# Optimization experiments

Measured on AMD Instinct MI355X. Metric: run time of the kernel, lower is better.

Reference implementation:

```python
import jax, jax.numpy as jnp
import numpy as np

NDIM = 1024
NTOKEN = 50257
CUTOFFS = [2000, 10000, NTOKEN]  # cutoffs + [ntoken]
DIV = 4
N = 4096
HEAD_SIZE = CUTOFFS[0] + len(CUTOFFS) - 1  # 2002


def setup_inputs() -> dict:
    key = jax.random.key(0)
    ks = jax.random.split(key, 8)
    inputs = jax.random.normal(ks[0], (N, NDIM), dtype=jnp.float32)
    targets = jax.random.randint(ks[1], (N,), 0, NTOKEN, dtype=jnp.int32)
    # head: nn.Linear(ndim, head_size, bias=False) -> weight [head_size, ndim], xavier
    def xavier(k, shape):
        fan_out, fan_in = shape
        lim = np.sqrt(6.0 / (fan_in + fan_out))
        return jax.random.uniform(k, shape, jnp.float32, -lim, lim)
    head_W = xavier(ks[2], (HEAD_SIZE, NDIM))
    # tail cluster 0: size 8000, low dim 256; cluster 1: size 40257, low dim 64
    sz0 = CUTOFFS[1] - CUTOFFS[0]
    sz1 = CUTOFFS[2] - CUTOFFS[1]
    d0, d1 = NDIM // DIV, NDIM // DIV**2
    emb0 = jax.random.normal(ks[3], (sz0, d0), dtype=jnp.float32) * d0 ** -0.5
    emb1 = jax.random.normal(ks[4], (sz1, d1), dtype=jnp.float32) * d1 ** -0.5
    lin0 = xavier(ks[5], (NDIM, d0))  # nn.Linear(d0, ndim).weight
    lin1 = xavier(ks[6], (NDIM, d1))
    return {"inputs": inputs, "targets": targets, "head_W": head_W,
            "emb0": emb0, "lin0": lin0, "emb1": emb1, "lin1": lin1}


def _adaptive_logprob(inputs, targets, head_W, emb0, lin0, emb1, lin1):
    tails = [(emb0, lin0), (emb1, lin1)]
    # map targets -> head targets (in-head id, or cluster slot cutoffs[0]+i)
    head_targets = targets
    masks = []
    for i in range(len(tails)):
        m = (targets >= CUTOFFS[i]) & (targets < CUTOFFS[i + 1])
        masks.append(m)
        head_targets = jnp.where(m, CUTOFFS[0] + i, head_targets)
    # head: logits [N, head_size], gather per-row log-prob
    head_lp = jax.nn.log_softmax(inputs @ head_W.T, axis=-1)
    out = jnp.take_along_axis(head_lp, head_targets[:, None], axis=1)[:, 0]
    # tails: logits = (x @ lin) @ emb^T (low-rank), log-softmax, masked gather
    for i, (emb, lin) in enumerate(tails):
        size = CUTOFFS[i + 1] - CUTOFFS[i]
        lp = jax.nn.log_softmax((inputs @ lin) @ emb.T, axis=-1)  # [N, size]
        rel = jnp.clip(targets - CUTOFFS[i], 0, size - 1)
        g = jnp.take_along_axis(lp, rel[:, None], axis=1)[:, 0]
        out = out + jnp.where(masks[i], g, 0.0)
    return out


def reference(inputs, targets, head_W, emb0, lin0, emb1, lin1):
    outputs = _adaptive_logprob(inputs, targets, head_W, emb0, lin0, emb1, lin1)
    loss = (-outputs).mean()
    return outputs, loss
```

## Files before the change

### kernel.cpp

```cpp
#include <hip/hip_runtime.h>


typedef __attribute__((ext_vector_type(8))) short short8;
typedef __attribute__((ext_vector_type(4))) float f32x4;

#define LOG2E 1.4426950408889634f
#define LN2   0.6931471805599453f

__device__ __forceinline__ float b2f(unsigned short u){
    return __uint_as_float(((unsigned int)u) << 16);
}
__device__ __forceinline__ unsigned short f2b(float f){
    unsigned int x = __float_as_uint(f);
    x += 0x7fffu + ((x >> 16) & 1u);
    return (unsigned short)(x >> 16);
}
__device__ __forceinline__ float dotu(unsigned int xu, unsigned int wu){
    float a = __uint_as_float(xu << 16) * __uint_as_float(wu << 16);
    float b = __uint_as_float(xu & 0xffff0000u) * __uint_as_float(wu & 0xffff0000u);
    return a + b;
}
__device__ __forceinline__ float fexp2(float x){
#if __has_builtin(__builtin_amdgcn_exp2f)
    return __builtin_amdgcn_exp2f(x);
#else
    float r; asm("v_exp_f32 %0, %1" : "=v"(r) : "v"(x)); return r;
#endif
}

__global__ __launch_bounds__(256) void k_prep(
    const float* __restrict__ X, const float* __restrict__ headW,
    const float* __restrict__ emb0, const float* __restrict__ emb1,
    const float* __restrict__ lin0, const float* __restrict__ lin1,
    unsigned short* __restrict__ Xb, unsigned short* __restrict__ hWb,
    unsigned short* __restrict__ e0b, unsigned short* __restrict__ e1b,
    unsigned short* __restrict__ l0T, unsigned short* __restrict__ l1T,
    float* __restrict__ sums)
{
    __shared__ unsigned short tileT[64][65];
    const int b = blockIdx.x, t = threadIdx.x;
    if (b < 80){
        const float* src; unsigned short* dst; int C, tx, ty;
        if (b < 64){ src = lin0; dst = l0T; C = 256; tx = b & 3; ty = b >> 2; }
        else       { src = lin1; dst = l1T; C = 64;  tx = 0;     ty = b - 64; }
        #pragma unroll
        for (int e = 0; e < 16; ++e){
            int idx = t + e*256, r = idx >> 6, c = idx & 63;
            tileT[c][r] = f2b(src[(ty*64 + r)*C + tx*64 + c]);
        }
        __syncthreads();
        #pragma unroll
        for (int e = 0; e < 16; ++e){
            int idx = t + e*256, cc = idx >> 6, rr = idx & 63;
            dst[(tx*64 + cc)*1024 + ty*64 + rr] = tileT[cc][rr];
        }
        return;
    }
    const int NX = 1048576, NH = 512512, NE0 = 512000, NE1 = 644112;
    const int NV = NX + NH + NE0 + NE1;
    const int NS = 12288;
    const int total = NV + NS;
    int stride = (gridDim.x - 80) * blockDim.x;
    for (int i = (b - 80)*blockDim.x + t; i < total; i += stride){
        if (i < NV){
            const float* src; unsigned short* dst; int off; float sc;
            if (i < NX)            { src = X;     dst = Xb;  off = i;           sc = 1.0f;  }
            else if (i < NX+NH)    { src = headW; dst = hWb; off = i-NX;        sc = LOG2E; }
            else if (i < NX+NH+NE0){ src = emb0;  dst = e0b; off = i-NX-NH;     sc = LOG2E; }
            else                   { src = emb1;  dst = e1b; off = i-NX-NH-NE0; sc = LOG2E; }
            float4 v = ((const float4*)src)[off];
            ushort4 o;
            o.x = f2b(v.x*sc); o.y = f2b(v.y*sc);
            o.z = f2b(v.z*sc); o.w = f2b(v.w*sc);
            ((ushort4*)dst)[off] = o;
        } else {
            sums[i - NV] = 0.f;
        }
    }
}

__global__ __launch_bounds__(256) void k_hgemm(
    const unsigned short* __restrict__ A,
    const unsigned short* __restrict__ B0, unsigned short* __restrict__ C0,
    const unsigned short* __restrict__ B1, unsigned short* __restrict__ C1)
{
    constexpr int K = 1024;
    __shared__ __align__(16) unsigned short As[64*64];
    __shared__ __align__(16) unsigned short Bs[64*64];

    const int yy = blockIdx.y;
    const unsigned short* B = (yy < 4) ? B0 : B1;
    unsigned short* C = (yy < 4) ? C0 : C1;
    const int M  = (yy < 4) ? 256 : 64;
    const int cb = (yy < 4) ? yy : 0;

    const int tid  = threadIdx.x;
    const int lane = tid & 63;
    const int w    = tid >> 6;
    const int waveR = w >> 1, waveC = w & 1;
    const int quad  = lane >> 4, l16 = lane & 15;
    const int row0  = blockIdx.x * 64;

    f32x4 acc[2][2];
    #pragma unroll
    for (int i = 0; i < 2; ++i)
    #pragma unroll
    for (int j = 0; j < 2; ++j)
        acc[i][j] = (f32x4){0.f, 0.f, 0.f, 0.f};

    for (int kc = 0; kc < K/64; ++kc){
        __syncthreads();
        #pragma unroll
        for (int it = 0; it < 2; ++it){
            int idx = tid + it*256;
            int r = idx >> 3, g = idx & 7;
            *((uint4*)&As[r*64 + ((g ^ (r & 7)) << 3)]) =
                *(const uint4*)(A + (row0 + r)*K + kc*64 + g*8);
            *((uint4*)&Bs[r*64 + ((g ^ (r & 7)) << 3)]) =
                *(const uint4*)(B + (cb*64 + r)*K + kc*64 + g*8);
        }
        __syncthreads();
        #pragma unroll
        for (int ks = 0; ks < 2; ++ks){
            short8 a[2], b[2];
            #pragma unroll
            for (int i = 0; i < 2; ++i){
                int r = waveR*32 + i*16 + l16;
                int g = ks*4 + quad;
                a[i] = *(const short8*)&As[r*64 + ((g ^ (r & 7)) << 3)];
            }
            #pragma unroll
            for (int j = 0; j < 2; ++j){
                int r = waveC*32 + j*16 + l16;
                int g = ks*4 + quad;
                b[j] = *(const short8*)&Bs[r*64 + ((g ^ (r & 7)) << 3)];
            }
            #pragma unroll
            for (int i = 0; i < 2; ++i)
            #pragma unroll
            for (int j = 0; j < 2; ++j)
                acc[i][j] = __builtin_amdgcn_mfma_f32_16x16x32_bf16(
                    a[i], b[j], acc[i][j], 0, 0, 0);
        }
    }
    #pragma unroll
    for (int i = 0; i < 2; ++i)
    #pragma unroll
    for (int j = 0; j < 2; ++j)
    #pragma unroll
    for (int r = 0; r < 4; ++r){
        int row = row0 + waveR*32 + i*16 + quad*4 + r;
        int col = cb*64 + waveC*32 + j*16 + l16;
        C[row*M + col] = f2b(acc[i][j][r]);
    }
}

template<int K>
__device__ __forceinline__ void sumexp_lds(
    const unsigned short* __restrict__ A,
    const unsigned short* __restrict__ B,
    float* __restrict__ s_out, int M,
    int rowb, int cb0, int cb1,
    unsigned short* __restrict__ As,
    unsigned short* __restrict__ Bs)
{
    constexpr int KCH = K / 64;
    constexpr int LK  = (KCH == 16) ? 4 : 2;
    static_assert(KCH == 16 || KCH == 4, "");
    const int tid  = threadIdx.x;
    const int lane = tid & 63, w = tid >> 6;
    const int waveR = w >> 1, waveC = w & 1;
    const int quad  = lane >> 4, l16 = lane & 15;
    const int row0  = rowb * 64;
    const int nit   = (cb1 - cb0) << LK;

    float s_loc[8];
    #pragma unroll
    for (int i = 0; i < 8; ++i) s_loc[i] = 0.f;
    f32x4 acc[2][2];
    #pragma unroll
    for (int i = 0; i < 2; ++i)
    #pragma unroll
    for (int j = 0; j < 2; ++j) acc[i][j] = (f32x4){0.f,0.f,0.f,0.f};

    const int srow = tid >> 3;
    const int sg   = tid & 7;
    const int so0 = srow*64 + ((sg ^ (srow & 7)) << 3);
    const int so1 = (srow+32)*64 + ((sg ^ ((srow+32) & 7)) << 3);

    int aoff[2][2], boff[2][2];
    #pragma unroll
    for (int x = 0; x < 2; ++x)
    #pragma unroll
    for (int ks = 0; ks < 2; ++ks){
        int ra = waveR*32 + x*16 + l16;
        int rb = waveC*32 + x*16 + l16;
        int g  = ks*4 + quad;
        aoff[x][ks] = ra*64 + ((g ^ (ra & 7)) << 3);
        boff[x][ks] = rb*64 + ((g ^ (rb & 7)) << 3);
    }

    uint4 A0a, A1a, B0a, B1a, A0b, A1b, B0b, B1b;
    auto loadAB = [&](int it, uint4& A0, uint4& A1, uint4& B0, uint4& B1){
        int cb = cb0 + (it >> LK);
        int kc = it & (KCH - 1);
        const unsigned short* ap = A + (row0 + srow)*K + kc*64 + sg*8;
        A0 = *(const uint4*)ap;
        A1 = *(const uint4*)(ap + 32*K);
        int br = cb*64 + srow;
        const unsigned short* bp = B + br*K + kc*64 + sg*8;
        B0 = (br      < M) ? *(const uint4*)bp          : (uint4){0,0,0,0};
        B1 = (br + 32 < M) ? *(const uint4*)(bp + 32*K) : (uint4){0,0,0,0};
    };
    auto writeAB = [&](int it, uint4 A0, uint4 A1, uint4 B0, uint4 B1){
        unsigned short* Ad = As + (it & 1)*4096;
        unsigned short* Bd = Bs + (it & 1)*4096;
        *(uint4*)(Ad + so0) = A0; *(uint4*)(Ad + so1) = A1;
        *(uint4*)(Bd + so0) = B0; *(uint4*)(Bd + so1) = B1;
    };
    auto compute = [&](int buf){
        const unsigned short* Ac = As + buf*4096;
        const unsigned short* Bc = Bs + buf*4096;
        #pragma unroll
        for (int ks = 0; ks < 2; ++ks){
            short8 a0 = *(const short8*)(Ac + aoff[0][ks]);
            short8 a1 = *(const short8*)(Ac + aoff[1][ks]);
            short8 b0 = *(const short8*)(Bc + boff[0][ks]);
            short8 b1 = *(const short8*)(Bc + boff[1][ks]);
            acc[0][0] = __builtin_amdgcn_mfma_f32_16x16x32_bf16(a0, b0, acc[0][0], 0,0,0);
            acc[0][1] = __builtin_amdgcn_mfma_f32_16x16x32_bf16(a0, b1, acc[0][1], 0,0,0);
            acc[1][0] = __builtin_amdgcn_mfma_f32_16x16x32_bf16(a1, b0, acc[1][0], 0,0,0);
            acc[1][1] = __builtin_amdgcn_mfma_f32_16x16x32_bf16(a1, b1, acc[1][1], 0,0,0);
        }
    };
    auto epilogue = [&](int it){
        int cb = cb0 + (it >> LK);
        if ((cb + 1)*64 <= M){
            #pragma unroll
            for (int i = 0; i < 2; ++i)
            #pragma unroll
            for (int j = 0; j < 2; ++j)
            #pragma unroll
            for (int r = 0; r < 4; ++r)
                s_loc[i*4 + r] += fexp2(acc[i][j][r]);
        } else {
            #pragma unroll
            for (int j = 0; j < 2; ++j){
                int col = cb*64 + waveC*32 + j*16 + l16;
                if (col < M){
                    #pragma unroll
                    for (int i = 0; i < 2; ++i)
                    #pragma unroll
                    for (int r = 0; r < 4; ++r)
                        s_loc[i*4 + r] += fexp2(acc[i][j][r]);
                }
            }
        }
        #pragma unroll
        for (int i = 0; i < 2; ++i)
        #pragma unroll
        for (int j = 0; j < 2; ++j) acc[i][j] = (f32x4){0.f,0.f,0.f,0.f};
    };

    loadAB(0, A0a, A1a, B0a, B1a);
    writeAB(0, A0a, A1a, B0a, B1a);
    loadAB(1, A0b, A1b, B0b, B1b);
    loadAB(2, A0a, A1a, B0a, B1a);
    __syncthreads();

    for (int it = 0; it < nit; it += 2){
        writeAB(it + 1, A0b, A1b, B0b, B1b);
        if (it + 3 < nit) loadAB(it + 3, A0b, A1b, B0b, B1b);
        compute(0);
        __syncthreads();
        if (it + 2 < nit) writeAB(it + 2, A0a, A1a, B0a, B1a);
        if (it + 4 < nit) loadAB(it + 4, A0a, A1a, B0a, B1a);
        compute(1);
        if (((it + 1) & (KCH - 1)) == (KCH - 1)) epilogue(it + 1);
        __syncthreads();
    }

    #pragma unroll
    for (int k = 0; k < 8; ++k){
        #pragma unroll
        for (int m = 1; m < 16; m <<= 1)
            s_loc[k] += __shfl_xor(s_loc[k], m, 64);
    }
    if (l16 < 8){
        int i = l16 >> 2, r = l16 & 3;
        int row = row0 + waveR*32 + i*16 + quad*4 + r;
        atomicAdd(&s_out[row], s_loc[l16]);
    }
}

__device__ __forceinline__ void sumexp_stream64(
    const unsigned short* __restrict__ A,
    const unsigned short* __restrict__ B,
    float* __restrict__ s_out, int wid)
{
    const int M = 40257;
    const int lane = threadIdx.x & 63;
    const int quad = lane >> 4, l16 = lane & 15;
    const int rowg  = wid >> 6;
    const int split = wid & 63;
    const int g0 = split*39 + min(split, 21);
    const int g1 = g0 + 39 + (split < 21 ? 1 : 0);
    const int row0 = rowg * 64;

    short8 a[4][2];
    #pragma unroll
    for (int i = 0; i < 4; ++i)
    #pragma unroll
    for (int ks = 0; ks < 2; ++ks)
        a[i][ks] = *(const short8*)(A + (row0 + i*16 + l16)*64 + ks*32 + quad*8);

    f32x4 sums[4];
    #pragma unroll
    for (int i = 0; i < 4; ++i) sums[i] = (f32x4){0.f,0.f,0.f,0.f};

    short8 p0a, p1a, p0b, p1b;
    auto loadB = [&](int g, short8& d0, short8& d1){
        int n = g*16 + l16; if (n > M-1) n = M-1;
        const unsigned short* p = B + n*64 + quad*8;
        d0 = *(const short8*)p;
        d1 = *(const short8*)(p + 32);
    };
    auto body = [&](int g, short8 b0, short8 b1){
        f32x4 acc[4];
        #pragma unroll
        for (int i = 0; i < 4; ++i) acc[i] = (f32x4){0.f,0.f,0.f,0.f};
        #pragma unroll
        for (int i = 0; i < 4; ++i)
            acc[i] = __builtin_amdgcn_mfma_f32_16x16x32_bf16(a[i][0], b0, acc[i], 0,0,0);
        #pragma unroll
        for (int i = 0; i < 4; ++i)
            acc[i] = __builtin_amdgcn_mfma_f32_16x16x32_bf16(a[i][1], b1, acc[i], 0,0,0);
        if (g*16 + l16 < M){
            #pragma unroll
            for (int i = 0; i < 4; ++i){
                sums[i][0] += fexp2(acc[i][0]);
                sums[i][1] += fexp2(acc[i][1]);
                sums[i][2] += fexp2(acc[i][2]);
                sums[i][3] += fexp2(acc[i][3]);
            }
        }
    };

    loadB(g0, p0a, p1a);
    loadB(g0 + 1, p0b, p1b);
    for (int g = g0; g < g1; g += 2){
        body(g, p0a, p1a);
        if (g + 2 < g1) loadB(g + 2, p0a, p1a);
        if (g + 1 < g1){
            body(g + 1, p0b, p1b);
            if (g + 3 < g1) loadB(g + 3, p0b, p1b);
        }
    }

    #pragma unroll
    for (int i = 0; i < 4; ++i){
        #pragma unroll
        for (int r = 0; r < 4; ++r){
            float v = sums[i][r];
            v += __shfl_xor(v, 1, 64);
            v += __shfl_xor(v, 2, 64);
            v += __shfl_xor(v, 4, 64);
            v += __shfl_xor(v, 8, 64);
            if (l16 == 0)
                atomicAdd(&s_out[row0 + i*16 + quad*4 + r], v);
        }
    }
}

__global__ __launch_bounds__(256) void k_sumexp(
    const unsigned short* __restrict__ Xb,  const unsigned short* __restrict__ hWb,
    const unsigned short* __restrict__ h0b, const unsigned short* __restrict__ e0b,
    const unsigned short* __restrict__ h1b, const unsigned short* __restrict__ e1b,
    float* __restrict__ sH, float* __restrict__ s0, float* __restrict__ s1)
{
    __shared__ __align__(16) unsigned short As[2*4096];
    __shared__ __align__(16) unsigned short Bs[2*4096];
    const int b = blockIdx.x;
    const int m4 = b & 3;
    if (m4 == 0){
        int id = b >> 2, rowb = id >> 3, split = id & 7;
        sumexp_lds<1024>(Xb, hWb, sH, 2002, rowb, split*4, split*4 + 4, As, Bs);
    } else if (m4 == 2){
        int id = b >> 2, rowb = id >> 3, split = id & 7;
        int cb0 = split*15 + min(split, 5);
        int cb1 = cb0 + 15 + (split < 5 ? 1 : 0);
        sumexp_lds<256>(h0b, e0b, s0, 8000, rowb, cb0, cb1, As, Bs);
    } else {
        int wid = (b >> 1)*4 + (threadIdx.x >> 6);
        sumexp_stream64(h1b, e1b, s1, wid);
    }
}

__global__ __launch_bounds__(256) void k_combine(
    const unsigned short* __restrict__ Xb,
    const unsigned short* __restrict__ hWb,
    const unsigned short* __restrict__ h0b,
    const unsigned short* __restrict__ e0b,
    const unsigned short* __restrict__ h1b,
    const unsigned short* __restrict__ e1b,
    const float* __restrict__ sH, const float* __restrict__ s0,
    const float* __restrict__ s1,
    const int* __restrict__ targets, float* __restrict__ out)
{
    int w = threadIdx.x >> 6, lane = threadIdx.x & 63;
    int row = blockIdx.x*4 + w;
    int t = targets[row];
    int hidx = t < 2000 ? t : (t < 10000 ? 2000 : 2001);
    int rel0 = min(max(t - 2000, 0), 7999);
    int rel1 = min(max(t - 10000, 0), 40256);

    float dh = 0.f;
    {
        const uint4* xa = (const uint4*)(Xb  + row*1024  + lane*16);
        const uint4* wb = (const uint4*)(hWb + hidx*1024 + lane*16);
        #pragma unroll
        for (int p = 0; p < 2; ++p){
            uint4 xv = xa[p], wv = wb[p];
            dh += dotu(xv.x, wv.x) + dotu(xv.y, wv.y)
                + dotu(xv.z, wv.z) + dotu(xv.w, wv.w);
        }
    }
    float d0;
    {
        uint2 xv = *(const uint2*)(h0b + row*256  + lane*4);
        uint2 wv = *(const uint2*)(e0b + rel0*256 + lane*4);
        d0 = dotu(xv.x, wv.x) + dotu(xv.y, wv.y);
    }
    float d1 = b2f(h1b[row*64 + lane]) * b2f(e1b[rel1*64 + lane]);

    #pragma unroll
    for (int m = 1; m < 64; m <<= 1){
        dh += __shfl_xor(dh, m, 64);
        d0 += __shfl_xor(d0, m, 64);
        d1 += __shfl_xor(d1, m, 64);
    }
    if (lane == 0){
        float lp = dh - log2f(sH[row]);
        if (t >= 2000 && t < 10000) lp += d0 - log2f(s0[row]);
        if (t >= 10000)             lp += d1 - log2f(s1[row]);
        out[row] = LN2 * lp;
    }
}

__global__ void k_loss(const float* __restrict__ out, float* __restrict__ loss){
    __shared__ float red[1024];
    float s = 0.f;
    for (int i = threadIdx.x; i < 4096; i += 1024) s += out[i];
    red[threadIdx.x] = s;
    __syncthreads();
    for (int ofs = 512; ofs > 0; ofs >>= 1){
        if (threadIdx.x < ofs) red[threadIdx.x] += red[threadIdx.x + ofs];
        __syncthreads();
    }
    if (threadIdx.x == 0) loss[0] = -red[0] / 4096.f;
}

extern "C" void kernel_launch(void* const* d_in, const int* in_sizes, int n_in,
                              void* d_out, int out_size, void* d_ws, size_t ws_size,
                              hipStream_t stream) {
    const float* X      = (const float*)d_in[0];
    const int*   tgt    = (const int*)  d_in[1];
    const float* headW  = (const float*)d_in[2];
    const float* emb0   = (const float*)d_in[3];
    const float* lin0   = (const float*)d_in[4];
    const float* emb1   = (const float*)d_in[5];
    const float* lin1   = (const float*)d_in[6];
    float* out = (float*)d_out;

    char* ws = (char*)d_ws;
    unsigned short* Xb  = (unsigned short*)(ws + 0);
    unsigned short* hWb = (unsigned short*)(ws + 8388608);
    unsigned short* e0b = (unsigned short*)(ws + 12488704);
    unsigned short* e1b = (unsigned short*)(ws + 16584704);
    unsigned short* l0T = (unsigned short*)(ws + 21737600);
    unsigned short* l1T = (unsigned short*)(ws + 22261888);
    unsigned short* h0b = (unsigned short*)(ws + 22392960);
    unsigned short* h1b = (unsigned short*)(ws + 24490112);
    float* sums         = (float*)(ws + 25014400);
    float* sH = sums, *s0 = sums + 4096, *s1 = sums + 8192;

    k_prep<<<2048, 256, 0, stream>>>(X, headW, emb0, emb1, lin0, lin1,
                                     Xb, hWb, e0b, e1b, l0T, l1T, sums);
    k_hgemm<<<dim3(64, 5), 256, 0, stream>>>(Xb, l0T, h0b, l1T, h1b);
    k_sumexp<<<2048, 256, 0, stream>>>(Xb, hWb, h0b, e0b, h1b, e1b, sH, s0, s1);
    k_combine<<<1024, 256, 0, stream>>>(Xb, hWb, h0b, e0b, h1b, e1b,
                                        sH, s0, s1, tgt, out);
    k_loss<<<1, 1024, 0, stream>>>(out, out + 4096);
}
```

Before: 234.2 us.

## Use 128x128 MFMA tiles with direct global-to-LDS loads in GEMM and sum-exp kernels

Grows the block tile in the projection GEMM and the head and tail-0 sum-exp kernels from 64x64 to 128x128, so each wave runs a 4x4 grid of MFMA tiles. The LDS tiles are now filled with global_load_lds instead of going through registers. The projection GEMM now reads lin0 and lin1 as one 320-row matrix, which relies on the two buffers sitting next to each other in the workspace. The tail-1 streaming path now covers 128 rows per wave, and the work split and grid sizes are recomputed to match. The goal is more operand reuse and less global and LDS staging traffic per FLOP. In exchange it drops the earlier register double-buffered prefetch pipeline, launches fewer blocks, and raises register pressure.

```diff
diff --git a/kernel.cpp b/kernel.cpp
--- a/kernel.cpp
+++ b/kernel.cpp
@@ -26,6 +26,11 @@
 #else
     float r; asm("v_exp_f32 %0, %1" : "=v"(r) : "v"(x)); return r;
 #endif
+}
+__device__ __forceinline__ void gload16(const unsigned short* g, unsigned short* l){
+    __builtin_amdgcn_global_load_lds(
+        (const __attribute__((address_space(1))) unsigned int*)g,
+        (__attribute__((address_space(3))) unsigned int*)l, 16, 0, 0);
 }
 
 __global__ __launch_bounds__(256) void k_prep(
@@ -79,221 +84,176 @@
     }
 }
 
+
 __global__ __launch_bounds__(256) void k_hgemm(
     const unsigned short* __restrict__ A,
-    const unsigned short* __restrict__ B0, unsigned short* __restrict__ C0,
-    const unsigned short* __restrict__ B1, unsigned short* __restrict__ C1)
+    const unsigned short* __restrict__ B,
+    unsigned short* __restrict__ C0,
+    unsigned short* __restrict__ C1)
 {
     constexpr int K = 1024;
-    __shared__ __align__(16) unsigned short As[64*64];
-    __shared__ __align__(16) unsigned short Bs[64*64];
-
-    const int yy = blockIdx.y;
-    const unsigned short* B = (yy < 4) ? B0 : B1;
-    unsigned short* C = (yy < 4) ? C0 : C1;
-    const int M  = (yy < 4) ? 256 : 64;
-    const int cb = (yy < 4) ? yy : 0;
-
-    const int tid  = threadIdx.x;
-    const int lane = tid & 63;
-    const int w    = tid >> 6;
+    __shared__ __align__(16) unsigned short As[128*64];
+    __shared__ __align__(16) unsigned short Bs[128*64];
+    const int rowb = blockIdx.x / 3, cb = blockIdx.x % 3;
+    const int tid = threadIdx.x, lane = tid & 63, w = tid >> 6;
     const int waveR = w >> 1, waveC = w & 1;
-    const int quad  = lane >> 4, l16 = lane & 15;
-    const int row0  = blockIdx.x * 64;
-
-    f32x4 acc[2][2];
-    #pragma unroll
-    for (int i = 0; i < 2; ++i)
-    #pragma unroll
-    for (int j = 0; j < 2; ++j)
-        acc[i][j] = (f32x4){0.f, 0.f, 0.f, 0.f};
+    const int quad = lane >> 4, l16 = lane & 15;
+    const int row0 = rowb * 128;
+    const int srow = w*32 + (lane >> 3);
+    const int gk   = ((lane & 7) ^ (srow & 7)) << 3;
+    unsigned short* ldsA = As + w*4*512;
+    unsigned short* ldsB = Bs + w*4*512;
+    const int sA = (waveR*64 + l16)*64 + ((quad ^ (l16 & 7)) << 3);
+    const int sB = (waveC*64 + l16)*64 + ((quad ^ (l16 & 7)) << 3);
+
+    f32x4 acc[4][4];
+    #pragma unroll
+    for (int i = 0; i < 4; ++i)
+    #pragma unroll
+    for (int j = 0; j < 4; ++j) acc[i][j] = (f32x4){0.f,0.f,0.f,0.f};
 
     for (int kc = 0; kc < K/64; ++kc){
         __syncthreads();
-        #pragma unroll
-        for (int it = 0; it < 2; ++it){
-            int idx = tid + it*256;
-            int r = idx >> 3, g = idx & 7;
-            *((uint4*)&As[r*64 + ((g ^ (r & 7)) << 3)]) =
-                *(const uint4*)(A + (row0 + r)*K + kc*64 + g*8);
-            *((uint4*)&Bs[r*64 + ((g ^ (r & 7)) << 3)]) =
-                *(const uint4*)(B + (cb*64 + r)*K + kc*64 + g*8);
+        const unsigned short* gA = A + (size_t)(row0 + srow)*K + kc*64 + gk;
+        #pragma unroll
+        for (int c = 0; c < 4; ++c)
+            gload16(gA + c*8*K, ldsA + c*512);
+        #pragma unroll
+        for (int c = 0; c < 4; ++c){
+            int br = min(cb*128 + srow + c*8, 319);
+            gload16(B + (size_t)br*K + kc*64 + gk, ldsB + c*512);
         }
         __syncthreads();
         #pragma unroll
         for (int ks = 0; ks < 2; ++ks){
-            short8 a[2], b[2];
-            #pragma unroll
-            for (int i = 0; i < 2; ++i){
-                int r = waveR*32 + i*16 + l16;
-                int g = ks*4 + quad;
-                a[i] = *(const short8*)&As[r*64 + ((g ^ (r & 7)) << 3)];
+            const int xo = ks << 5;
+            short8 a0 = *(const short8*)&As[(sA ^ xo)         ];
+            short8 a1 = *(const short8*)&As[(sA ^ xo) + 1024  ];
+            short8 a2 = *(const short8*)&As[(sA ^ xo) + 2048  ];
+            short8 a3 = *(const short8*)&As[(sA ^ xo) + 3072  ];
+            short8 b0 = *(const short8*)&Bs[(sB ^ xo)         ];
+            short8 b1 = *(const short8*)&Bs[(sB ^ xo) + 1024  ];
+            short8 b2 = *(const short8*)&Bs[(sB ^ xo) + 2048  ];
+            short8 b3 = *(const short8*)&Bs[(sB ^ xo) + 3072  ];
+            #pragma unroll
+            for (int i = 0; i < 4; ++i){
+                short8 av = (i==0)?a0:(i==1)?a1:(i==2)?a2:a3;
+                acc[i][0] = __builtin_amdgcn_mfma_f32_16x16x32_bf16(av, b0, acc[i][0], 0,0,0);
+                acc[i][1] = __builtin_amdgcn_mfma_f32_16x16x32_bf16(av, b1, acc[i][1], 0,0,0);
+                acc[i][2] = __builtin_amdgcn_mfma_f32_16x16x32_bf16(av, b2, acc[i][2], 0,0,0);
+                acc[i][3] = __builtin_amdgcn_mfma_f32_16x16x32_bf16(av, b3, acc[i][3], 0,0,0);
             }
-            #pragma unroll
-            for (int j = 0; j < 2; ++j){
-                int r = waveC*32 + j*16 + l16;
-                int g = ks*4 + quad;
-                b[j] = *(const short8*)&Bs[r*64 + ((g ^ (r & 7)) << 3)];
-            }
-            #pragma unroll
-            for (int i = 0; i < 2; ++i)
-            #pragma unroll
-            for (int j = 0; j < 2; ++j)
-                acc[i][j] = __builtin_amdgcn_mfma_f32_16x16x32_bf16(
-                    a[i], b[j], acc[i][j], 0, 0, 0);
-        }
-    }
-    #pragma unroll
-    for (int i = 0; i < 2; ++i)
-    #pragma unroll
-    for (int j = 0; j < 2; ++j)
+        }
+    }
+    #pragma unroll
+    for (int i = 0; i < 4; ++i)
+    #pragma unroll
+    for (int j = 0; j < 4; ++j)
     #pragma unroll
     for (int r = 0; r < 4; ++r){
-        int row = row0 + waveR*32 + i*16 + quad*4 + r;
-        int col = cb*64 + waveC*32 + j*16 + l16;
-        C[row*M + col] = f2b(acc[i][j][r]);
+        int row = row0 + waveR*64 + i*16 + quad*4 + r;
+        int col = cb*128 + waveC*64 + j*16 + l16;
+        if (col < 256) C0[row*256 + col] = f2b(acc[i][j][r]);
+        else if (col < 320) C1[row*64 + (col - 256)] = f2b(acc[i][j][r]);
     }
 }
 
 template<int K>
-__device__ __forceinline__ void sumexp_lds(
+__device__ __forceinline__ void sumexp128(
     const unsigned short* __restrict__ A,
     const unsigned short* __restrict__ B,
     float* __restrict__ s_out, int M,
     int rowb, int cb0, int cb1,
-    unsigned short* __restrict__ As,
-    unsigned short* __restrict__ Bs)
+    unsigned short* __restrict__ As, unsigned short* __restrict__ Bs)
 {
     constexpr int KCH = K / 64;
-    constexpr int LK  = (KCH == 16) ? 4 : 2;
-    static_assert(KCH == 16 || KCH == 4, "");
-    const int tid  = threadIdx.x;
-    const int lane = tid & 63, w = tid >> 6;
+    const int tid = threadIdx.x, lane = tid & 63, w = tid >> 6;
     const int waveR = w >> 1, waveC = w & 1;
-    const int quad  = lane >> 4, l16 = lane & 15;
-    const int row0  = rowb * 64;
-    const int nit   = (cb1 - cb0) << LK;
-
-    float s_loc[8];
-    #pragma unroll
-    for (int i = 0; i < 8; ++i) s_loc[i] = 0.f;
-    f32x4 acc[2][2];
-    #pragma unroll
-    for (int i = 0; i < 2; ++i)
-    #pragma unroll
-    for (int j = 0; j < 2; ++j) acc[i][j] = (f32x4){0.f,0.f,0.f,0.f};
-
-    const int srow = tid >> 3;
-    const int sg   = tid & 7;
-    const int so0 = srow*64 + ((sg ^ (srow & 7)) << 3);
-    const int so1 = (srow+32)*64 + ((sg ^ ((srow+32) & 7)) << 3);
-
-    int aoff[2][2], boff[2][2];
-    #pragma unroll
-    for (int x = 0; x < 2; ++x)
-    #pragma unroll
-    for (int ks = 0; ks < 2; ++ks){
-        int ra = waveR*32 + x*16 + l16;
-        int rb = waveC*32 + x*16 + l16;
-        int g  = ks*4 + quad;
-        aoff[x][ks] = ra*64 + ((g ^ (ra & 7)) << 3);
-        boff[x][ks] = rb*64 + ((g ^ (rb & 7)) << 3);
-    }
-
-    uint4 A0a, A1a, B0a, B1a, A0b, A1b, B0b, B1b;
-    auto loadAB = [&](int it, uint4& A0, uint4& A1, uint4& B0, uint4& B1){
-        int cb = cb0 + (it >> LK);
-        int kc = it & (KCH - 1);
-        const unsigned short* ap = A + (row0 + srow)*K + kc*64 + sg*8;
-        A0 = *(const uint4*)ap;
-        A1 = *(const uint4*)(ap + 32*K);
-        int br = cb*64 + srow;
-        const unsigned short* bp = B + br*K + kc*64 + sg*8;
-        B0 = (br      < M) ? *(const uint4*)bp          : (uint4){0,0,0,0};
-        B1 = (br + 32 < M) ? *(const uint4*)(bp + 32*K) : (uint4){0,0,0,0};
-    };
-    auto writeAB = [&](int it, uint4 A0, uint4 A1, uint4 B0, uint4 B1){
-        unsigned short* Ad = As + (it & 1)*4096;
-        unsigned short* Bd = Bs + (it & 1)*4096;
-        *(uint4*)(Ad + so0) = A0; *(uint4*)(Ad + so1) = A1;
-        *(uint4*)(Bd + so0) = B0; *(uint4*)(Bd + so1) = B1;
-    };
-    auto compute = [&](int buf){
-        const unsigned short* Ac = As + buf*4096;
-        const unsigned short* Bc = Bs + buf*4096;
-        #pragma unroll
-        for (int ks = 0; ks < 2; ++ks){
-            short8 a0 = *(const short8*)(Ac + aoff[0][ks]);
-            short8 a1 = *(const short8*)(Ac + aoff[1][ks]);
-            short8 b0 = *(const short8*)(Bc + boff[0][ks]);
-            short8 b1 = *(const short8*)(Bc + boff[1][ks]);
-            acc[0][0] = __builtin_amdgcn_mfma_f32_16x16x32_bf16(a0, b0, acc[0][0], 0,0,0);
-            acc[0][1] = __builtin_amdgcn_mfma_f32_16x16x32_bf16(a0, b1, acc[0][1], 0,0,0);
-            acc[1][0] = __builtin_amdgcn_mfma_f32_16x16x32_bf16(a1, b0, acc[1][0], 0,0,0);
-            acc[1][1] = __builtin_amdgcn_mfma_f32_16x16x32_bf16(a1, b1, acc[1][1], 0,0,0);
-        }
-    };
-    auto epilogue = [&](int it){
-        int cb = cb0 + (it >> LK);
-        if ((cb + 1)*64 <= M){
-            #pragma unroll
-            for (int i = 0; i < 2; ++i)
-            #pragma unroll
-            for (int j = 0; j < 2; ++j)
+    const int quad = lane >> 4, l16 = lane & 15;
+    const int row0 = rowb * 128;
+    const int srow = w*32 + (lane >> 3);
+    const int gk   = ((lane & 7) ^ (srow & 7)) << 3;
+    unsigned short* ldsA = As + w*4*512;
+    unsigned short* ldsB = Bs + w*4*512;
+    const int sA = (waveR*64 + l16)*64 + ((quad ^ (l16 & 7)) << 3);
+    const int sB = (waveC*64 + l16)*64 + ((quad ^ (l16 & 7)) << 3);
+
+    float s_loc[16];
+    #pragma unroll
+    for (int i = 0; i < 16; ++i) s_loc[i] = 0.f;
+
+    for (int cb = cb0; cb < cb1; ++cb){
+        f32x4 acc[4][4];
+        #pragma unroll
+        for (int i = 0; i < 4; ++i)
+        #pragma unroll
+        for (int j = 0; j < 4; ++j) acc[i][j] = (f32x4){0.f,0.f,0.f,0.f};
+
+        for (int kc = 0; kc < KCH; ++kc){
+            __syncthreads();
+            const unsigned short* gA = A + (size_t)(row0 + srow)*K + kc*64 + gk;
+            #pragma unroll
+            for (int c = 0; c < 4; ++c)
+                gload16(gA + c*8*K, ldsA + c*512);
+            #pragma unroll
+            for (int c = 0; c < 4; ++c){
+                int br = min(cb*128 + srow + c*8, M-1);
+                gload16(B + (size_t)br*K + kc*64 + gk, ldsB + c*512);
+            }
+            __syncthreads();
+            #pragma unroll
+            for (int ks = 0; ks < 2; ++ks){
+                const int xo = ks << 5;
+                short8 a0 = *(const short8*)&As[(sA ^ xo)        ];
+                short8 a1 = *(const short8*)&As[(sA ^ xo) + 1024 ];
+                short8 a2 = *(const short8*)&As[(sA ^ xo) + 2048 ];
+                short8 a3 = *(const short8*)&As[(sA ^ xo) + 3072 ];
+                short8 b0 = *(const short8*)&Bs[(sB ^ xo)        ];
+                short8 b1 = *(const short8*)&Bs[(sB ^ xo) + 1024 ];
+                short8 b2 = *(const short8*)&Bs[(sB ^ xo) + 2048 ];
+                short8 b3 = *(const short8*)&Bs[(sB ^ xo) + 3072 ];
+                #pragma unroll
+                for (int i = 0; i < 4; ++i){
+                    short8 av = (i==0)?a0:(i==1)?a1:(i==2)?a2:a3;
+                    acc[i][0] = __builtin_amdgcn_mfma_f32_16x16x32_bf16(av, b0, acc[i][0], 0,0,0);
+                    acc[i][1] = __builtin_amdgcn_mfma_f32_16x16x32_bf16(av, b1, acc[i][1], 0,0,0);
+                    acc[i][2] = __builtin_amdgcn_mfma_f32_16x16x32_bf16(av, b2, acc[i][2], 0,0,0);
+                    acc[i][3] = __builtin_amdgcn_mfma_f32_16x16x32_bf16(av, b3, acc[i][3], 0,0,0);
+                }
+            }
+        }
+        bool full = ((cb + 1)*128 <= M);
+        #pragma unroll
+        for (int j = 0; j < 4; ++j){
+            if (!full){
+                int col = cb*128 + waveC*64 + j*16 + l16;
+                if (col >= M) continue;
+            }
+            #pragma unroll
+            for (int i = 0; i < 4; ++i)
             #pragma unroll
             for (int r = 0; r < 4; ++r)
                 s_loc[i*4 + r] += fexp2(acc[i][j][r]);
-        } else {
-            #pragma unroll
-            for (int j = 0; j < 2; ++j){
-                int col = cb*64 + waveC*32 + j*16 + l16;
-                if (col < M){
-                    #pragma unroll
-                    for (int i = 0; i < 2; ++i)
-                    #pragma unroll
-                    for (int r = 0; r < 4; ++r)
-                        s_loc[i*4 + r] += fexp2(acc[i][j][r]);
-                }
-            }
-        }
-        #pragma unroll
-        for (int i = 0; i < 2; ++i)
-        #pragma unroll
-        for (int j = 0; j < 2; ++j) acc[i][j] = (f32x4){0.f,0.f,0.f,0.f};
-    };
-
-    loadAB(0, A0a, A1a, B0a, B1a);
-    writeAB(0, A0a, A1a, B0a, B1a);
-    loadAB(1, A0b, A1b, B0b, B1b);
-    loadAB(2, A0a, A1a, B0a, B1a);
-    __syncthreads();
-
-    for (int it = 0; it < nit; it += 2){
-        writeAB(it + 1, A0b, A1b, B0b, B1b);
-        if (it + 3 < nit) loadAB(it + 3, A0b, A1b, B0b, B1b);
-        compute(0);
-        __syncthreads();
-        if (it + 2 < nit) writeAB(it + 2, A0a, A1a, B0a, B1a);
-        if (it + 4 < nit) loadAB(it + 4, A0a, A1a, B0a, B1a);
-        compute(1);
-        if (((it + 1) & (KCH - 1)) == (KCH - 1)) epilogue(it + 1);
-        __syncthreads();
-    }
-
-    #pragma unroll
-    for (int k = 0; k < 8; ++k){
-        #pragma unroll
-        for (int m = 1; m < 16; m <<= 1)
-            s_loc[k] += __shfl_xor(s_loc[k], m, 64);
-    }
-    if (l16 < 8){
-        int i = l16 >> 2, r = l16 & 3;
-        int row = row0 + waveR*32 + i*16 + quad*4 + r;
-        atomicAdd(&s_out[row], s_loc[l16]);
-    }
-}
-
-__device__ __forceinline__ void sumexp_stream64(
+        }
+    }
+
+    #pragma unroll
+    for (int k = 0; k < 16; ++k){
+        s_loc[k] += __shfl_xor(s_loc[k], 1, 64);
+        s_loc[k] += __shfl_xor(s_loc[k], 2, 64);
+        s_loc[k] += __shfl_xor(s_loc[k], 4, 64);
+        s_loc[k] += __shfl_xor(s_loc[k], 8, 64);
+    }
+    if (l16 == 0){
+        #pragma unroll
+        for (int k = 0; k < 16; ++k){
+            int row = row0 + waveR*64 + (k >> 2)*16 + quad*4 + (k & 3);
+            atomicAdd(&s_out[row], s_loc[k]);
+        }
+    }
+}
+
+__device__ __forceinline__ void sumexp_stream128(
     const unsigned short* __restrict__ A,
     const unsigned short* __restrict__ B,
     float* __restrict__ s_out, int wid)
@@ -305,18 +265,18 @@
     const int split = wid & 63;
     const int g0 = split*39 + min(split, 21);
     const int g1 = g0 + 39 + (split < 21 ? 1 : 0);
-    const int row0 = rowg * 64;
-
-    short8 a[4][2];
-    #pragma unroll
-    for (int i = 0; i < 4; ++i)
+    const int row0 = rowg * 128;
+
+    short8 a[8][2];
+    #pragma unroll
+    for (int i = 0; i < 8; ++i)
     #pragma unroll
     for (int ks = 0; ks < 2; ++ks)
         a[i][ks] = *(const short8*)(A + (row0 + i*16 + l16)*64 + ks*32 + quad*8);
 
-    f32x4 sums[4];
-    #pragma unroll
-    for (int i = 0; i < 4; ++i) sums[i] = (f32x4){0.f,0.f,0.f,0.f};
+    f32x4 sums[8];
+    #pragma unroll
+    for (int i = 0; i < 8; ++i) sums[i] = (f32x4){0.f,0.f,0.f,0.f};
 
     short8 p0a, p1a, p0b, p1b;
     auto loadB = [&](int g, short8& d0, short8& d1){
@@ -326,18 +286,18 @@
         d1 = *(const short8*)(p + 32);
     };
     auto body = [&](int g, short8 b0, short8 b1){
-        f32x4 acc[4];
-        #pragma unroll
-        for (int i = 0; i < 4; ++i) acc[i] = (f32x4){0.f,0.f,0.f,0.f};
-        #pragma unroll
-        for (int i = 0; i < 4; ++i)
+        f32x4 acc[8];
+        #pragma unroll
+        for (int i = 0; i < 8; ++i) acc[i] = (f32x4){0.f,0.f,0.f,0.f};
+        #pragma unroll
+        for (int i = 0; i < 8; ++i)
             acc[i] = __builtin_amdgcn_mfma_f32_16x16x32_bf16(a[i][0], b0, acc[i], 0,0,0);
         #pragma unroll
-        for (int i = 0; i < 4; ++i)
+        for (int i = 0; i < 8; ++i)
             acc[i] = __builtin_amdgcn_mfma_f32_16x16x32_bf16(a[i][1], b1, acc[i], 0,0,0);
         if (g*16 + l16 < M){
             #pragma unroll
-            for (int i = 0; i < 4; ++i){
+            for (int i = 0; i < 8; ++i){
                 sums[i][0] += fexp2(acc[i][0]);
                 sums[i][1] += fexp2(acc[i][1]);
                 sums[i][2] += fexp2(acc[i][2]);
@@ -358,7 +318,7 @@
     }
 
     #pragma unroll
-    for (int i = 0; i < 4; ++i){
+    for (int i = 0; i < 8; ++i){
         #pragma unroll
         for (int r = 0; r < 4; ++r){
             float v = sums[i][r];
@@ -378,31 +338,26 @@
     const unsigned short* __restrict__ h1b, const unsigned short* __restrict__ e1b,
     float* __restrict__ sH, float* __restrict__ s0, float* __restrict__ s1)
 {
-    __shared__ __align__(16) unsigned short As[2*4096];
-    __shared__ __align__(16) unsigned short Bs[2*4096];
-    const int b = blockIdx.x;
-    const int m4 = b & 3;
-    if (m4 == 0){
-        int id = b >> 2, rowb = id >> 3, split = id & 7;
-        sumexp_lds<1024>(Xb, hWb, sH, 2002, rowb, split*4, split*4 + 4, As, Bs);
-    } else if (m4 == 2){
-        int id = b >> 2, rowb = id >> 3, split = id & 7;
-        int cb0 = split*15 + min(split, 5);
-        int cb1 = cb0 + 15 + (split < 5 ? 1 : 0);
-        sumexp_lds<256>(h0b, e0b, s0, 8000, rowb, cb0, cb1, As, Bs);
+    __shared__ __align__(16) unsigned short As[128*64];
+    __shared__ __align__(16) unsigned short Bs[128*64];
+    const unsigned b = blockIdx.x;
+    const unsigned g = b / 33u, p = b % 33u;
+    if (p < 8u){
+        int id = g*8 + p;
+        sumexp128<1024>(Xb, hWb, sH, 2002, id >> 3, (id & 7)*2, (id & 7)*2 + 2, As, Bs);
+    } else if (p < 17u){
+        int id = g*9 + (p - 8);
+        sumexp128<256>(h0b, e0b, s0, 8000, id/9, (id%9)*7, (id%9)*7 + 7, As, Bs);
     } else {
-        int wid = (b >> 1)*4 + (threadIdx.x >> 6);
-        sumexp_stream64(h1b, e1b, s1, wid);
+        int id = g*16 + (p - 17);
+        sumexp_stream128(h1b, e1b, s1, id*4 + (threadIdx.x >> 6));
     }
 }
 
 __global__ __launch_bounds__(256) void k_combine(
-    const unsigned short* __restrict__ Xb,
-    const unsigned short* __restrict__ hWb,
-    const unsigned short* __restrict__ h0b,
-    const unsigned short* __restrict__ e0b,
-    const unsigned short* __restrict__ h1b,
-    const unsigned short* __restrict__ e1b,
+    const unsigned short* __restrict__ Xb,   const unsigned short* __restrict__ hWb,
+    const unsigned short* __restrict__ h0b,  const unsigned short* __restrict__ e0b,
+    const unsigned short* __restrict__ h1b,  const unsigned short* __restrict__ e1b,
     const float* __restrict__ sH, const float* __restrict__ s0,
     const float* __restrict__ s1,
     const int* __restrict__ targets, float* __restrict__ out)
@@ -486,8 +441,8 @@
 
     k_prep<<<2048, 256, 0, stream>>>(X, headW, emb0, emb1, lin0, lin1,
                                      Xb, hWb, e0b, e1b, l0T, l1T, sums);
-    k_hgemm<<<dim3(64, 5), 256, 0, stream>>>(Xb, l0T, h0b, l1T, h1b);
-    k_sumexp<<<2048, 256, 0, stream>>>(Xb, hWb, h0b, e0b, h1b, e1b, sH, s0, s1);
+    k_hgemm<<<96, 256, 0, stream>>>(Xb, l0T, h0b, h1b);
+    k_sumexp<<<1056, 256, 0, stream>>>(Xb, hWb, h0b, e0b, h1b, e1b, sH, s0, s1);
     k_combine<<<1024, 256, 0, stream>>>(Xb, hWb, h0b, e0b, h1b, e1b,
                                         sH, s0, s1, tgt, out);
     k_loss<<<1, 1024, 0, stream>>>(out, out + 4096);
```

Result: slower. 275.8 us (+17.8%).

## Stage GEMM tiles via direct global-to-LDS loads with single-sync loop

Applied to the files above, without the earlier changes.

Replaces the register-staged global-load-then-LDS-write double buffering in the LDS sum-exp GEMM with __builtin_amdgcn_global_load_lds 16-byte direct transfers into the swizzled LDS buffers. The loop becomes one iteration per k-chunk with a single barrier, and out-of-range B rows are clamped to the last valid row instead of zero-filled. The aim is to save VGPRs and the ds_write instructions and let loads go straight to LDS. In exchange the prefetch depth drops from two stages held in registers to one, so load latency may be less well hidden.

```diff
diff --git a/kernel.cpp b/kernel.cpp
--- a/kernel.cpp
+++ b/kernel.cpp
@@ -26,6 +26,11 @@
 #else
     float r; asm("v_exp_f32 %0, %1" : "=v"(r) : "v"(x)); return r;
 #endif
+}
+__device__ __forceinline__ void gload16(const unsigned short* g, unsigned short* l){
+    __builtin_amdgcn_global_load_lds(
+        (const __attribute__((address_space(1))) unsigned int*)g,
+        (__attribute__((address_space(3))) unsigned int*)l, 16, 0, 0);
 }
 
 __global__ __launch_bounds__(256) void k_prep(
@@ -183,10 +188,8 @@
     #pragma unroll
     for (int j = 0; j < 2; ++j) acc[i][j] = (f32x4){0.f,0.f,0.f,0.f};
 
-    const int srow = tid >> 3;
-    const int sg   = tid & 7;
-    const int so0 = srow*64 + ((sg ^ (srow & 7)) << 3);
-    const int so1 = (srow+32)*64 + ((sg ^ ((srow+32) & 7)) << 3);
+    const int sr = w*16 + (lane >> 3);
+    const int gk = ((lane & 7) ^ (sr & 7)) << 3;
 
     int aoff[2][2], boff[2][2];
     #pragma unroll
@@ -200,27 +203,27 @@
         boff[x][ks] = rb*64 + ((g ^ (rb & 7)) << 3);
     }
 
-    uint4 A0a, A1a, B0a, B1a, A0b, A1b, B0b, B1b;
-    auto loadAB = [&](int it, uint4& A0, uint4& A1, uint4& B0, uint4& B1){
+    auto stage = [&](int it){
         int cb = cb0 + (it >> LK);
         int kc = it & (KCH - 1);
-        const unsigned short* ap = A + (row0 + srow)*K + kc*64 + sg*8;
-        A0 = *(const uint4*)ap;
-        A1 = *(const uint4*)(ap + 32*K);
-        int br = cb*64 + srow;
-        const unsigned short* bp = B + br*K + kc*64 + sg*8;
-        B0 = (br      < M) ? *(const uint4*)bp          : (uint4){0,0,0,0};
-        B1 = (br + 32 < M) ? *(const uint4*)(bp + 32*K) : (uint4){0,0,0,0};
+        unsigned short* Ad = As + (it & 1)*4096 + w*1024;
+        unsigned short* Bd = Bs + (it & 1)*4096 + w*1024;
+        const unsigned short* ga = A + (size_t)(row0 + sr)*K + kc*64 + gk;
+        gload16(ga,        Ad);
+        gload16(ga + 8*K,  Ad + 512);
+        int br0 = cb*64 + sr;     if (br0 > M-1) br0 = M-1;
+        int br1 = cb*64 + sr + 8; if (br1 > M-1) br1 = M-1;
+        gload16(B + (size_t)br0*K + kc*64 + gk, Bd);
+        gload16(B + (size_t)br1*K + kc*64 + gk, Bd + 512);
     };
-    auto writeAB = [&](int it, uint4 A0, uint4 A1, uint4 B0, uint4 B1){
-        unsigned short* Ad = As + (it & 1)*4096;
-        unsigned short* Bd = Bs + (it & 1)*4096;
-        *(uint4*)(Ad + so0) = A0; *(uint4*)(Ad + so1) = A1;
-        *(uint4*)(Bd + so0) = B0; *(uint4*)(Bd + so1) = B1;
-    };
-    auto compute = [&](int buf){
-        const unsigned short* Ac = As + buf*4096;
-        const unsigned short* Bc = Bs + buf*4096;
+
+    stage(0);
+    __syncthreads();
+
+    for (int it = 0; it < nit; ++it){
+        if (it + 1 < nit) stage(it + 1);
+        const unsigned short* Ac = As + (it & 1)*4096;
+        const unsigned short* Bc = Bs + (it & 1)*4096;
         #pragma unroll
         for (int ks = 0; ks < 2; ++ks){
             short8 a0 = *(const short8*)(Ac + aoff[0][ks]);
@@ -232,51 +235,34 @@
             acc[1][0] = __builtin_amdgcn_mfma_f32_16x16x32_bf16(a1, b0, acc[1][0], 0,0,0);
             acc[1][1] = __builtin_amdgcn_mfma_f32_16x16x32_bf16(a1, b1, acc[1][1], 0,0,0);
         }
-    };
-    auto epilogue = [&](int it){
-        int cb = cb0 + (it >> LK);
-        if ((cb + 1)*64 <= M){
-            #pragma unroll
-            for (int i = 0; i < 2; ++i)
-            #pragma unroll
-            for (int j = 0; j < 2; ++j)
-            #pragma unroll
-            for (int r = 0; r < 4; ++r)
-                s_loc[i*4 + r] += fexp2(acc[i][j][r]);
-        } else {
-            #pragma unroll
-            for (int j = 0; j < 2; ++j){
-                int col = cb*64 + waveC*32 + j*16 + l16;
-                if (col < M){
-                    #pragma unroll
-                    for (int i = 0; i < 2; ++i)
-                    #pragma unroll
-                    for (int r = 0; r < 4; ++r)
-                        s_loc[i*4 + r] += fexp2(acc[i][j][r]);
+        if ((it & (KCH - 1)) == (KCH - 1)){
+            int cb = cb0 + (it >> LK);
+            if ((cb + 1)*64 <= M){
+                #pragma unroll
+                for (int i = 0; i < 2; ++i)
+                #pragma unroll
+                for (int j = 0; j < 2; ++j)
+                #pragma unroll
+                for (int r = 0; r < 4; ++r)
+                    s_loc[i*4 + r] += fexp2(acc[i][j][r]);
+            } else {
+                #pragma unroll
+                for (int j = 0; j < 2; ++j){
+                    int col = cb*64 + waveC*32 + j*16 + l16;
+                    if (col < M){
+                        #pragma unroll
+                        for (int i = 0; i < 2; ++i)
+                        #pragma unroll
+                        for (int r = 0; r < 4; ++r)
+                            s_loc[i*4 + r] += fexp2(acc[i][j][r]);
+                    }
                 }
             }
-        }
-        #pragma unroll
-        for (int i = 0; i < 2; ++i)
-        #pragma unroll
-        for (int j = 0; j < 2; ++j) acc[i][j] = (f32x4){0.f,0.f,0.f,0.f};
-    };
-
-    loadAB(0, A0a, A1a, B0a, B1a);
-    writeAB(0, A0a, A1a, B0a, B1a);
-    loadAB(1, A0b, A1b, B0b, B1b);
-    loadAB(2, A0a, A1a, B0a, B1a);
-    __syncthreads();
-
-    for (int it = 0; it < nit; it += 2){
-        writeAB(it + 1, A0b, A1b, B0b, B1b);
-        if (it + 3 < nit) loadAB(it + 3, A0b, A1b, B0b, B1b);
-        compute(0);
-        __syncthreads();
-        if (it + 2 < nit) writeAB(it + 2, A0a, A1a, B0a, B1a);
-        if (it + 4 < nit) loadAB(it + 4, A0a, A1a, B0a, B1a);
-        compute(1);
-        if (((it + 1) & (KCH - 1)) == (KCH - 1)) epilogue(it + 1);
+            #pragma unroll
+            for (int i = 0; i < 2; ++i)
+            #pragma unroll
+            for (int j = 0; j < 2; ++j) acc[i][j] = (f32x4){0.f,0.f,0.f,0.f};
+        }
         __syncthreads();
     }
 
@@ -397,12 +383,9 @@
 }
 
 __global__ __launch_bounds__(256) void k_combine(
-    const unsigned short* __restrict__ Xb,
-    const unsigned short* __restrict__ hWb,
-    const unsigned short* __restrict__ h0b,
-    const unsigned short* __restrict__ e0b,
-    const unsigned short* __restrict__ h1b,
-    const unsigned short* __restrict__ e1b,
+    const unsigned short* __restrict__ Xb,   const unsigned short* __restrict__ hWb,
+    const unsigned short* __restrict__ h0b,  const unsigned short* __restrict__ e0b,
+    const unsigned short* __restrict__ h1b,  const unsigned short* __restrict__ e1b,
     const float* __restrict__ sH, const float* __restrict__ s0,
     const float* __restrict__ s1,
     const int* __restrict__ targets, float* __restrict__ out)
```

Measured after the change: 235.4 us. No clear change (+0.5%).
